# Performance work log

Hardware: AMD Instinct MI355X
Metric: run time of the kernel (lower is better)

## Reference

```python
import jax, jax.numpy as jnp
import numpy as np

N = 50000      # nodes
E = 800000     # edges
G = 512        # graphs
H = 256        # hidden_dim
T = 32         # tag embedding dim
L = 4          # num_layers
EPS = 1e-5


def setup_inputs() -> dict:
    key = jax.random.key(0)
    ks = jax.random.split(key, 16)
    x = jax.random.randint(ks[0], (N,), 0, 100)
    tags = jax.random.randint(ks[1], (N,), 0, 3)
    edge_index = jax.random.randint(ks[2], (2, E), 0, N)
    batch = jnp.sort(jax.random.randint(ks[3], (N,), 0, G))
    s = 1.0 / np.sqrt(H)
    atom_emb = jax.random.normal(ks[4], (100, H), jnp.float32)
    tag_emb = jax.random.normal(ks[5], (3, T), jnp.float32)
    Wp = jax.random.normal(ks[6], (H + T, H), jnp.float32) * (1.0 / np.sqrt(H + T))
    bp = jnp.zeros((H,), jnp.float32)
    gcn_W = jax.random.normal(ks[7], (L, H, H), jnp.float32) * s
    gcn_b = jnp.zeros((L, H), jnp.float32)
    bn_g = jnp.ones((L, H), jnp.float32)
    bn_b = jnp.zeros((L, H), jnp.float32)
    W1 = jax.random.normal(ks[8], (H, H // 2), jnp.float32) * s
    b1 = jnp.zeros((H // 2,), jnp.float32)
    W2 = jax.random.normal(ks[9], (H // 2, 1), jnp.float32) * (1.0 / np.sqrt(H // 2))
    b2 = jnp.zeros((1,), jnp.float32)
    return dict(x=x, tags=tags, edge_index=edge_index, batch=batch,
                atom_emb=atom_emb, tag_emb=tag_emb, Wp=Wp, bp=bp,
                gcn_W=gcn_W, gcn_b=gcn_b, bn_g=bn_g, bn_b=bn_b,
                W1=W1, b1=b1, W2=W2, b2=b2)


def _gcn_conv(h, W, b, src, dst, dinv):
    # PyG GCNConv: x' = W x, symmetric normalization with self-loops.
    hw = h @ W                                   # [N, H]
    norm = dinv[src] * dinv[dst]                 # [E]
    msg = hw[src] * norm[:, None]                # [E, H]  (gather)
    agg = jax.ops.segment_sum(msg, dst, num_segments=N)  # scatter-add
    agg = agg + hw * (dinv * dinv)[:, None]      # self-loop term
    return agg + b


def _batch_norm(x, g, b):
    mu = jnp.mean(x, axis=0)
    var = jnp.var(x, axis=0)
    return (x - mu) * jax.lax.rsqrt(var + EPS) * g + b


def reference(x, tags, edge_index, batch, atom_emb, tag_emb, Wp, bp,
              gcn_W, gcn_b, bn_g, bn_b, W1, b1, W2, b2):
    src, dst = edge_index[0], edge_index[1]
    # degree with self-loops (gcn_norm counts on the dst/col index)
    deg = jax.ops.segment_sum(jnp.ones((E,), jnp.float32), dst, num_segments=N) + 1.0
    dinv = jax.lax.rsqrt(deg)

    h = jnp.concatenate([atom_emb[x], tag_emb[tags]], axis=1) @ Wp + bp  # [N, H]
    for l in range(L):
        res = h
        h = _gcn_conv(h, gcn_W[l], gcn_b[l], src, dst, dinv)
        h = jax.nn.relu(_batch_norm(h, bn_g[l], bn_b[l]))
        h = h + res                                  # dropout is identity in eval

    # global mean pool over graphs
    sums = jax.ops.segment_sum(h, batch, num_segments=G)
    cnts = jax.ops.segment_sum(jnp.ones((N,), jnp.float32), batch, num_segments=G)
    pooled = sums / jnp.maximum(cnts, 1.0)[:, None]  # [G, H]

    hid = jax.nn.relu(pooled @ W1 + b1)
    energy = hid @ W2 + b2                           # [G, 1]
    return energy.squeeze(-1)
```

## Files before the change

### kernel.cpp

```cpp
#include <hip/hip_runtime.h>
#include <hip/hip_bf16.h>

#define NN 50000
#define EE 800000
#define GG 512
#define HH 256
#define TT 32
#define LL 4
#define EPSF 1e-5f

typedef __attribute__((ext_vector_type(8))) short short8;
typedef __attribute__((ext_vector_type(4))) float float4v;

__device__ inline unsigned short f2b(float f) {
    unsigned u = __float_as_uint(f);
    unsigned r = (u + 0x7FFFu + ((u >> 16) & 1u)) >> 16;
    return (unsigned short)r;
}
__device__ inline float4 bf4_to_f4(ushort4 u) {
    float4 f;
    f.x = __uint_as_float((unsigned)u.x << 16);
    f.y = __uint_as_float((unsigned)u.y << 16);
    f.z = __uint_as_float((unsigned)u.z << 16);
    f.w = __uint_as_float((unsigned)u.w << 16);
    return f;
}

__global__ void k_degree(const int* __restrict__ dst, int* __restrict__ cnt, int E) {
    int e = blockIdx.x * 256 + threadIdx.x;
    if (e < E) atomicAdd(&cnt[dst[e]], 1);
}

__global__ void k_dinv(const int* __restrict__ cnt, float* __restrict__ dinv, int N) {
    int i = blockIdx.x * 256 + threadIdx.x;
    if (i < N) dinv[i] = rsqrtf((float)cnt[i] + 1.0f);
}

__global__ void k_scan1(const int* __restrict__ cnt, int* __restrict__ incl,
                        int* __restrict__ bsum, int N) {
    __shared__ int s[1024];
    int i = blockIdx.x * 1024 + threadIdx.x;
    int v = (i < N) ? cnt[i] : 0;
    s[threadIdx.x] = v;
    __syncthreads();
    for (int off = 1; off < 1024; off <<= 1) {
        int t = (threadIdx.x >= off) ? s[threadIdx.x - off] : 0;
        __syncthreads();
        s[threadIdx.x] += t;
        __syncthreads();
    }
    if (i < N) incl[i] = s[threadIdx.x];
    if (threadIdx.x == 1023) bsum[blockIdx.x] = s[1023];
}

__global__ void k_scan2(int* __restrict__ bsum, int nb) {
    __shared__ int s[64];
    int v = (threadIdx.x < nb) ? bsum[threadIdx.x] : 0;
    s[threadIdx.x] = v;
    __syncthreads();
    for (int off = 1; off < 64; off <<= 1) {
        int t = (threadIdx.x >= off) ? s[threadIdx.x - off] : 0;
        __syncthreads();
        s[threadIdx.x] += t;
        __syncthreads();
    }
    if (threadIdx.x < nb) bsum[threadIdx.x] = s[threadIdx.x] - v;
}

__global__ void k_scan3(int* __restrict__ rs, const int* __restrict__ cnt,
                        const int* __restrict__ boff, int N) {
    int i = blockIdx.x * 256 + threadIdx.x;
    if (i < N) rs[i] = rs[i] + boff[i >> 10] - cnt[i];
}

__global__ void k_scatter(const int* __restrict__ src, const int* __restrict__ dst,
                          const int* __restrict__ rs, int* __restrict__ cur,
                          int* __restrict__ csr, int E) {
    int e = blockIdx.x * 256 + threadIdx.x;
    if (e >= E) return;
    int d = dst[e];
    int p = rs[d] + atomicAdd(&cur[d], 1);
    csr[p] = src[e];
}

__global__ void k_wprep(const float* __restrict__ W, unsigned short* __restrict__ Wt) {
    int l = blockIdx.y;
    int n = blockIdx.x * 4 + (threadIdx.x >> 6);
    int kq = (threadIdx.x & 63) * 4;
    const float* Wl = W + (size_t)l * HH * HH;
    ushort4 o;
    o.x = f2b(Wl[(size_t)(kq + 0) * HH + n]);
    o.y = f2b(Wl[(size_t)(kq + 1) * HH + n]);
    o.z = f2b(Wl[(size_t)(kq + 2) * HH + n]);
    o.w = f2b(Wl[(size_t)(kq + 3) * HH + n]);
    *(ushort4*)(Wt + (size_t)l * HH * HH + (size_t)n * HH + kq) = o;
}

__global__ void k_proj(const float* __restrict__ atom_emb, const float* __restrict__ tag_emb,
                       const float* __restrict__ Wp, const float* __restrict__ bp,
                       float* __restrict__ aref, float* __restrict__ tref) {
    int r = blockIdx.x;
    int j = threadIdx.x;
    if (r < 100) {
        float acc = bp[j];
        for (int k = 0; k < HH; ++k) acc += atom_emb[r * HH + k] * Wp[(size_t)k * HH + j];
        aref[r * HH + j] = acc;
    } else {
        int tr = r - 100;
        float acc = 0.f;
        for (int k = 0; k < TT; ++k) acc += tag_emb[tr * TT + k] * Wp[(size_t)(HH + k) * HH + j];
        tref[tr * HH + j] = acc;
    }
}

__global__ void k_h0(const int* __restrict__ x, const int* __restrict__ tags,
                     const float* __restrict__ aref, const float* __restrict__ tref,
                     float* __restrict__ h, unsigned short* __restrict__ hb, int N) {
    int n = blockIdx.x;
    int lane = threadIdx.x;
    float4 a = ((const float4*)(aref + (size_t)x[n] * HH))[lane];
    float4 t = ((const float4*)(tref + (size_t)tags[n] * HH))[lane];
    float4 r;
    r.x = a.x + t.x; r.y = a.y + t.y; r.z = a.z + t.z; r.w = a.w + t.w;
    ((float4*)(h + (size_t)n * HH))[lane] = r;
    ushort4 u;
    u.x = f2b(r.x); u.y = f2b(r.y); u.z = f2b(r.z); u.w = f2b(r.w);
    ((ushort4*)(hb + (size_t)n * HH))[lane] = u;
}

__global__ __launch_bounds__(256) void k_gemm(const unsigned short* __restrict__ hb,
                                              const unsigned short* __restrict__ Wt,
                                              const float* __restrict__ dinv,
                                              unsigned short* __restrict__ hwb, int M) {
    __shared__ unsigned short As[128][72];
    __shared__ unsigned short Bs[128][72];
    int t = threadIdx.x;
    int lane = t & 63, w = t >> 6;
    int wr = w >> 1, wc = w & 1;
    int l15 = lane & 15, l4 = lane >> 4;
    int row0 = blockIdx.y * 128, col0 = blockIdx.x * 128;
    float4v acc[4][4];
#pragma unroll
    for (int i = 0; i < 4; ++i)
#pragma unroll
        for (int j = 0; j < 4; ++j) acc[i][j] = (float4v)0.f;

    for (int k0 = 0; k0 < 256; k0 += 64) {
        if (k0) __syncthreads();
#pragma unroll
        for (int u = 0; u < 4; ++u) {
            int idx = u * 256 + t;
            int r = idx >> 3;
            int c = (idx & 7) * 8;
            *(uint4*)&As[r][c] = *(const uint4*)(hb + (size_t)(row0 + r) * 256 + k0 + c);
            *(uint4*)&Bs[r][c] = *(const uint4*)(Wt + (size_t)(col0 + r) * 256 + k0 + c);
        }
        __syncthreads();
#pragma unroll
        for (int kk = 0; kk < 64; kk += 32) {
            short8 a[4], b[4];
#pragma unroll
            for (int i = 0; i < 4; ++i)
                a[i] = *(const short8*)&As[wr * 64 + i * 16 + l15][kk + l4 * 8];
#pragma unroll
            for (int i = 0; i < 4; ++i)
                b[i] = *(const short8*)&Bs[wc * 64 + i * 16 + l15][kk + l4 * 8];
#pragma unroll
            for (int mi = 0; mi < 4; ++mi)
#pragma unroll
                for (int ni = 0; ni < 4; ++ni)
                    acc[mi][ni] = __builtin_amdgcn_mfma_f32_16x16x32_bf16(
                        a[mi], b[ni], acc[mi][ni], 0, 0, 0);
        }
    }
#pragma unroll
    for (int mi = 0; mi < 4; ++mi) {
        int mb = row0 + wr * 64 + mi * 16 + l4 * 4;
        float dv[4];
#pragma unroll
        for (int r = 0; r < 4; ++r) dv[r] = (mb + r < M) ? dinv[mb + r] : 0.f;
#pragma unroll
        for (int ni = 0; ni < 4; ++ni) {
            int n = col0 + wc * 64 + ni * 16 + l15;
#pragma unroll
            for (int r = 0; r < 4; ++r) {
                if (mb + r < M)
                    hwb[(size_t)(mb + r) * 256 + n] = f2b(acc[mi][ni][r] * dv[r]);
            }
        }
    }
}

__global__ void k_agg(const unsigned short* __restrict__ hwb, float* __restrict__ agg,
                      const int* __restrict__ csr, const int* __restrict__ rs,
                      const int* __restrict__ cnt, const float* __restrict__ dinv,
                      const float* __restrict__ bias, int N) {
    int wave = threadIdx.x >> 6;
    int lane = threadIdx.x & 63;
    int n = blockIdx.x * 4 + wave;
    if (n >= N) return;
    float dn = dinv[n];
    int e = rs[n];
    int end = e + cnt[n];
    float4 acc = bf4_to_f4(((const ushort4*)(hwb + (size_t)n * HH))[lane]);
    for (; e + 4 <= end; e += 4) {
        int s0 = csr[e], s1 = csr[e + 1], s2 = csr[e + 2], s3 = csr[e + 3];
        float4 m0 = bf4_to_f4(((const ushort4*)(hwb + (size_t)s0 * HH))[lane]);
        float4 m1 = bf4_to_f4(((const ushort4*)(hwb + (size_t)s1 * HH))[lane]);
        float4 m2 = bf4_to_f4(((const ushort4*)(hwb + (size_t)s2 * HH))[lane]);
        float4 m3 = bf4_to_f4(((const ushort4*)(hwb + (size_t)s3 * HH))[lane]);
        acc.x += (m0.x + m1.x) + (m2.x + m3.x);
        acc.y += (m0.y + m1.y) + (m2.y + m3.y);
        acc.z += (m0.z + m1.z) + (m2.z + m3.z);
        acc.w += (m0.w + m1.w) + (m2.w + m3.w);
    }
    for (; e < end; ++e) {
        int s = csr[e];
        float4 m = bf4_to_f4(((const ushort4*)(hwb + (size_t)s * HH))[lane]);
        acc.x += m.x; acc.y += m.y; acc.z += m.z; acc.w += m.w;
    }
    float4 b = ((const float4*)bias)[lane];
    float4 r;
    r.x = acc.x * dn + b.x; r.y = acc.y * dn + b.y;
    r.z = acc.z * dn + b.z; r.w = acc.w * dn + b.w;
    ((float4*)(agg + (size_t)n * HH))[lane] = r;
}

__global__ __launch_bounds__(256) void k_bnstats(const float4* __restrict__ agg,
                                                 float* __restrict__ colsum,
                                                 float* __restrict__ colsq, int N) {
    __shared__ float4 ssum[4][64];
    __shared__ float4 ssq[4][64];
    int lane = threadIdx.x & 63;
    int wv = threadIdx.x >> 6;
    int rows_per = (N + gridDim.x - 1) / gridDim.x;
    int r0 = blockIdx.x * rows_per;
    int r1 = r0 + rows_per; if (r1 > N) r1 = N;
    float4 s = make_float4(0.f, 0.f, 0.f, 0.f);
    float4 s2 = make_float4(0.f, 0.f, 0.f, 0.f);
    for (int r = r0 + wv; r < r1; r += 4) {
        float4 v = agg[(size_t)r * 64 + lane];
        s.x += v.x; s.y += v.y; s.z += v.z; s.w += v.w;
        s2.x += v.x * v.x; s2.y += v.y * v.y; s2.z += v.z * v.z; s2.w += v.w * v.w;
    }
    ssum[wv][lane] = s;
    ssq[wv][lane] = s2;
    __syncthreads();
    int j = lane * 4;
    if (wv == 0) {
        float4 a = ssum[0][lane], b = ssum[1][lane], c = ssum[2][lane], d = ssum[3][lane];
        atomicAdd(&colsum[j + 0], a.x + b.x + c.x + d.x);
        atomicAdd(&colsum[j + 1], a.y + b.y + c.y + d.y);
        atomicAdd(&colsum[j + 2], a.z + b.z + c.z + d.z);
        atomicAdd(&colsum[j + 3], a.w + b.w + c.w + d.w);
    } else if (wv == 1) {
        float4 a = ssq[0][lane], b = ssq[1][lane], c = ssq[2][lane], d = ssq[3][lane];
        atomicAdd(&colsq[j + 0], a.x + b.x + c.x + d.x);
        atomicAdd(&colsq[j + 1], a.y + b.y + c.y + d.y);
        atomicAdd(&colsq[j + 2], a.z + b.z + c.z + d.z);
        atomicAdd(&colsq[j + 3], a.w + b.w + c.w + d.w);
    }
}

__global__ void k_epi(const float4* __restrict__ agg, float4* __restrict__ h,
                      ushort4* __restrict__ hb,
                      const float4* __restrict__ colsum, const float4* __restrict__ colsq,
                      const float4* __restrict__ g4, const float4* __restrict__ b4,
                      int total, float invN) {
    int idx = blockIdx.x * 256 + threadIdx.x;
    if (idx >= total) return;
    int q = idx & 63;
    float4 a = agg[idx];
    float4 s = colsum[q], s2 = colsq[q], g = g4[q], b = b4[q];
    float4 hv = h[idx];
    float mu, var, v;
    mu = s.x * invN; var = s2.x * invN - mu * mu;
    v = (a.x - mu) * rsqrtf(var + EPSF) * g.x + b.x; hv.x += fmaxf(v, 0.f);
    mu = s.y * invN; var = s2.y * invN - mu * mu;
    v = (a.y - mu) * rsqrtf(var + EPSF) * g.y + b.y; hv.y += fmaxf(v, 0.f);
    mu = s.z * invN; var = s2.z * invN - mu * mu;
    v = (a.z - mu) * rsqrtf(var + EPSF) * g.z + b.z; hv.z += fmaxf(v, 0.f);
    mu = s.w * invN; var = s2.w * invN - mu * mu;
    v = (a.w - mu) * rsqrtf(var + EPSF) * g.w + b.w; hv.w += fmaxf(v, 0.f);
    h[idx] = hv;
    ushort4 u;
    u.x = f2b(hv.x); u.y = f2b(hv.y); u.z = f2b(hv.z); u.w = f2b(hv.w);
    hb[idx] = u;
}

__global__ void k_ginit(int* __restrict__ gstart, int G, int N) {
    int g = blockIdx.x * 256 + threadIdx.x;
    if (g <= G) gstart[g] = N;
}

__global__ void k_gbound(const int* __restrict__ batch, int* __restrict__ gstart, int N) {
    int n = blockIdx.x * 256 + threadIdx.x;
    if (n >= N) return;
    int b = batch[n];
    int prev = (n == 0) ? -1 : batch[n - 1];
    for (int g = prev + 1; g <= b; ++g) gstart[g] = n;
}

__global__ void k_pool(const float4* __restrict__ h, const int* __restrict__ gstart,
                       float* __restrict__ pooled) {
    __shared__ float4 sm[4][64];
    int g = blockIdx.x;
    int t = threadIdx.x;
    int lane = t & 63, wv = t >> 6;
    int s = gstart[g], e = gstart[g + 1];
    float4 acc = make_float4(0.f, 0.f, 0.f, 0.f);
    for (int n = s + wv; n < e; n += 4) {
        float4 v = h[(size_t)n * 64 + lane];
        acc.x += v.x; acc.y += v.y; acc.z += v.z; acc.w += v.w;
    }
    sm[wv][lane] = acc;
    __syncthreads();
    if (wv == 0) {
        float4 a = sm[0][lane], b = sm[1][lane], c = sm[2][lane], d = sm[3][lane];
        float inv = 1.0f / fmaxf((float)(e - s), 1.0f);
        float4 r;
        r.x = (a.x + b.x + c.x + d.x) * inv;
        r.y = (a.y + b.y + c.y + d.y) * inv;
        r.z = (a.z + b.z + c.z + d.z) * inv;
        r.w = (a.w + b.w + c.w + d.w) * inv;
        ((float4*)pooled)[(size_t)g * 64 + lane] = r;
    }
}

__global__ void k_head(const float* __restrict__ pooled,
                       const float* __restrict__ W1, const float* __restrict__ b1,
                       const float* __restrict__ W2, const float* __restrict__ b2,
                       float* __restrict__ out) {
    __shared__ float prow[256];
    __shared__ float hred[128];
    int g = blockIdx.x, t = threadIdx.x;
    prow[t] = pooled[(size_t)g * HH + t];
    prow[t + 128] = pooled[(size_t)g * HH + t + 128];
    __syncthreads();
    float acc = b1[t];
    for (int k = 0; k < HH; ++k) acc += prow[k] * W1[(size_t)k * 128 + t];
    float hid = fmaxf(acc, 0.f);
    hred[t] = hid * W2[t];
    __syncthreads();
    for (int off = 64; off > 0; off >>= 1) {
        if (t < off) hred[t] += hred[t + off];
        __syncthreads();
    }
    if (t == 0) out[g] = hred[0] + b2[0];
}

extern "C" void kernel_launch(void* const* d_in, const int* in_sizes, int n_in,
                              void* d_out, int out_size, void* d_ws, size_t ws_size,
                              hipStream_t stream) {
    const int* x        = (const int*)d_in[0];
    const int* tags     = (const int*)d_in[1];
    const int* ei       = (const int*)d_in[2];
    const int* batch    = (const int*)d_in[3];
    const float* atom_e = (const float*)d_in[4];
    const float* tag_e  = (const float*)d_in[5];
    const float* Wp     = (const float*)d_in[6];
    const float* bp     = (const float*)d_in[7];
    const float* gcn_W  = (const float*)d_in[8];
    const float* gcn_b  = (const float*)d_in[9];
    const float* bn_g   = (const float*)d_in[10];
    const float* bn_b   = (const float*)d_in[11];
    const float* W1     = (const float*)d_in[12];
    const float* b1     = (const float*)d_in[13];
    const float* W2     = (const float*)d_in[14];
    const float* b2     = (const float*)d_in[15];
    float* out = (float*)d_out;

    const int N = NN, E = EE, G = GG, H = HH;
    const int Mpad = ((N + 127) / 128) * 128;

    char* p = (char*)d_ws;
    auto alloc = [&](size_t bytes) {
        void* r = (void*)p;
        p += (bytes + 255) & ~(size_t)255;
        return r;
    };
    float* h    = (float*)alloc((size_t)N * H * 4);
    unsigned short* hb  = (unsigned short*)alloc((size_t)Mpad * H * 2);
    unsigned short* hwb = (unsigned short*)alloc((size_t)Mpad * H * 2);
    unsigned short* Wt  = (unsigned short*)alloc((size_t)LL * H * H * 2);
    float* agg  = (float*)alloc((size_t)N * H * 4);
    float* dinv = (float*)alloc((size_t)N * 4);
    int* cnt    = (int*)alloc((size_t)N * 4);
    int* rs     = (int*)alloc((size_t)N * 4);
    int* cur    = (int*)alloc((size_t)N * 4);
    int* csr    = (int*)alloc((size_t)E * 4);
    int* bsum   = (int*)alloc(64 * 4);
    float* aref = (float*)alloc(100 * (size_t)H * 4);
    float* tref = (float*)alloc(3 * (size_t)H * 4);
    float* cstat= (float*)alloc(2 * (size_t)H * 4);
    int* gstart = (int*)alloc((size_t)(G + 1) * 4);
    float* pooled = (float*)alloc((size_t)G * H * 4);

    const int* src = ei;
    const int* dst = ei + E;

    hipMemsetAsync(cnt, 0, (size_t)N * 4, stream);
    hipMemsetAsync(cur, 0, (size_t)N * 4, stream);

    k_degree<<<(E + 255) / 256, 256, 0, stream>>>(dst, cnt, E);
    k_dinv<<<(N + 255) / 256, 256, 0, stream>>>(cnt, dinv, N);

    int nb = (N + 1023) / 1024;
    k_scan1<<<nb, 1024, 0, stream>>>(cnt, rs, bsum, N);
    k_scan2<<<1, 64, 0, stream>>>(bsum, nb);
    k_scan3<<<(N + 255) / 256, 256, 0, stream>>>(rs, cnt, bsum, N);
    k_scatter<<<(E + 255) / 256, 256, 0, stream>>>(src, dst, rs, cur, csr, E);

    k_ginit<<<(G + 256) / 256, 256, 0, stream>>>(gstart, G, N);
    k_gbound<<<(N + 255) / 256, 256, 0, stream>>>(batch, gstart, N);

    k_wprep<<<dim3(64, LL), 256, 0, stream>>>(gcn_W, Wt);
    k_proj<<<103, 256, 0, stream>>>(atom_e, tag_e, Wp, bp, aref, tref);
    k_h0<<<N, 64, 0, stream>>>(x, tags, aref, tref, h, hb, N);

    for (int l = 0; l < LL; ++l) {
        k_gemm<<<dim3(2, Mpad / 128), 256, 0, stream>>>(
            hb, Wt + (size_t)l * H * H, dinv, hwb, N);
        k_agg<<<(N + 3) / 4, 256, 0, stream>>>(hwb, agg, csr, rs, cnt, dinv,
                                               gcn_b + (size_t)l * H, N);
        hipMemsetAsync(cstat, 0, 2 * (size_t)H * 4, stream);
        k_bnstats<<<512, 256, 0, stream>>>((const float4*)agg, cstat, cstat + H, N);
        k_epi<<<(N * 64 + 255) / 256, 256, 0, stream>>>(
            (const float4*)agg, (float4*)h, (ushort4*)hb,
            (const float4*)cstat, (const float4*)(cstat + H),
            (const float4*)(bn_g + (size_t)l * H), (const float4*)(bn_b + (size_t)l * H),
            N * 64, 1.0f / (float)N);
    }

    k_pool<<<G, 256, 0, stream>>>((const float4*)h, gstart, pooled);
    k_head<<<G, 128, 0, stream>>>(pooled, W1, b1, W2, b2, out);
}
```

Measured before the change: 941.8 us.

## Drop fp32 residual buffer, keep hidden state in bf16; unroll aggregation by eight

Removes the fp32 hidden-state array so the residual and pooling read the bf16 copy hb directly. This cuts a 51 MB fp32 read and write per layer in the epilogue, plus the fp32 writes in the initial embedding kernel. The neighbour aggregation loop also gains an 8-way unrolled path to keep more gather loads in flight. The trade-off is that the residual now accumulates in bf16 across layers, which loses precision.

```diff
diff --git a/kernel.cpp b/kernel.cpp
--- a/kernel.cpp
+++ b/kernel.cpp
@@ -115,16 +115,14 @@
 
 __global__ void k_h0(const int* __restrict__ x, const int* __restrict__ tags,
                      const float* __restrict__ aref, const float* __restrict__ tref,
-                     float* __restrict__ h, unsigned short* __restrict__ hb, int N) {
+                     unsigned short* __restrict__ hb, int N) {
     int n = blockIdx.x;
     int lane = threadIdx.x;
     float4 a = ((const float4*)(aref + (size_t)x[n] * HH))[lane];
     float4 t = ((const float4*)(tref + (size_t)tags[n] * HH))[lane];
-    float4 r;
-    r.x = a.x + t.x; r.y = a.y + t.y; r.z = a.z + t.z; r.w = a.w + t.w;
-    ((float4*)(h + (size_t)n * HH))[lane] = r;
     ushort4 u;
-    u.x = f2b(r.x); u.y = f2b(r.y); u.z = f2b(r.z); u.w = f2b(r.w);
+    u.x = f2b(a.x + t.x); u.y = f2b(a.y + t.y);
+    u.z = f2b(a.z + t.z); u.w = f2b(a.w + t.w);
     ((ushort4*)(hb + (size_t)n * HH))[lane] = u;
 }
 
@@ -203,6 +201,22 @@
     int e = rs[n];
     int end = e + cnt[n];
     float4 acc = bf4_to_f4(((const ushort4*)(hwb + (size_t)n * HH))[lane]);
+    for (; e + 8 <= end; e += 8) {
+        int s0 = csr[e],     s1 = csr[e + 1], s2 = csr[e + 2], s3 = csr[e + 3];
+        int s4 = csr[e + 4], s5 = csr[e + 5], s6 = csr[e + 6], s7 = csr[e + 7];
+        float4 m0 = bf4_to_f4(((const ushort4*)(hwb + (size_t)s0 * HH))[lane]);
+        float4 m1 = bf4_to_f4(((const ushort4*)(hwb + (size_t)s1 * HH))[lane]);
+        float4 m2 = bf4_to_f4(((const ushort4*)(hwb + (size_t)s2 * HH))[lane]);
+        float4 m3 = bf4_to_f4(((const ushort4*)(hwb + (size_t)s3 * HH))[lane]);
+        float4 m4 = bf4_to_f4(((const ushort4*)(hwb + (size_t)s4 * HH))[lane]);
+        float4 m5 = bf4_to_f4(((const ushort4*)(hwb + (size_t)s5 * HH))[lane]);
+        float4 m6 = bf4_to_f4(((const ushort4*)(hwb + (size_t)s6 * HH))[lane]);
+        float4 m7 = bf4_to_f4(((const ushort4*)(hwb + (size_t)s7 * HH))[lane]);
+        acc.x += ((m0.x + m1.x) + (m2.x + m3.x)) + ((m4.x + m5.x) + (m6.x + m7.x));
+        acc.y += ((m0.y + m1.y) + (m2.y + m3.y)) + ((m4.y + m5.y) + (m6.y + m7.y));
+        acc.z += ((m0.z + m1.z) + (m2.z + m3.z)) + ((m4.z + m5.z) + (m6.z + m7.z));
+        acc.w += ((m0.w + m1.w) + (m2.w + m3.w)) + ((m4.w + m5.w) + (m6.w + m7.w));
+    }
     for (; e + 4 <= end; e += 4) {
         int s0 = csr[e], s1 = csr[e + 1], s2 = csr[e + 2], s3 = csr[e + 3];
         float4 m0 = bf4_to_f4(((const ushort4*)(hwb + (size_t)s0 * HH))[lane]);
@@ -262,8 +276,7 @@
     }
 }
 
-__global__ void k_epi(const float4* __restrict__ agg, float4* __restrict__ h,
-                      ushort4* __restrict__ hb,
+__global__ void k_epi(const float4* __restrict__ agg, ushort4* __restrict__ hb,
                       const float4* __restrict__ colsum, const float4* __restrict__ colsq,
                       const float4* __restrict__ g4, const float4* __restrict__ b4,
                       int total, float invN) {
@@ -272,7 +285,7 @@
     int q = idx & 63;
     float4 a = agg[idx];
     float4 s = colsum[q], s2 = colsq[q], g = g4[q], b = b4[q];
-    float4 hv = h[idx];
+    float4 hv = bf4_to_f4(hb[idx]);
     float mu, var, v;
     mu = s.x * invN; var = s2.x * invN - mu * mu;
     v = (a.x - mu) * rsqrtf(var + EPSF) * g.x + b.x; hv.x += fmaxf(v, 0.f);
@@ -282,7 +295,6 @@
     v = (a.z - mu) * rsqrtf(var + EPSF) * g.z + b.z; hv.z += fmaxf(v, 0.f);
     mu = s.w * invN; var = s2.w * invN - mu * mu;
     v = (a.w - mu) * rsqrtf(var + EPSF) * g.w + b.w; hv.w += fmaxf(v, 0.f);
-    h[idx] = hv;
     ushort4 u;
     u.x = f2b(hv.x); u.y = f2b(hv.y); u.z = f2b(hv.z); u.w = f2b(hv.w);
     hb[idx] = u;
@@ -301,7 +313,7 @@
     for (int g = prev + 1; g <= b; ++g) gstart[g] = n;
 }
 
-__global__ void k_pool(const float4* __restrict__ h, const int* __restrict__ gstart,
+__global__ void k_pool(const unsigned short* __restrict__ hb, const int* __restrict__ gstart,
                        float* __restrict__ pooled) {
     __shared__ float4 sm[4][64];
     int g = blockIdx.x;
@@ -310,7 +322,7 @@
     int s = gstart[g], e = gstart[g + 1];
     float4 acc = make_float4(0.f, 0.f, 0.f, 0.f);
     for (int n = s + wv; n < e; n += 4) {
-        float4 v = h[(size_t)n * 64 + lane];
+        float4 v = bf4_to_f4(((const ushort4*)(hb + (size_t)n * HH))[lane]);
         acc.x += v.x; acc.y += v.y; acc.z += v.z; acc.w += v.w;
     }
     sm[wv][lane] = acc;
@@ -379,7 +391,6 @@
         p += (bytes + 255) & ~(size_t)255;
         return r;
     };
-    float* h    = (float*)alloc((size_t)N * H * 4);
     unsigned short* hb  = (unsigned short*)alloc((size_t)Mpad * H * 2);
     unsigned short* hwb = (unsigned short*)alloc((size_t)Mpad * H * 2);
     unsigned short* Wt  = (unsigned short*)alloc((size_t)LL * H * H * 2);
@@ -416,7 +427,7 @@
 
     k_wprep<<<dim3(64, LL), 256, 0, stream>>>(gcn_W, Wt);
     k_proj<<<103, 256, 0, stream>>>(atom_e, tag_e, Wp, bp, aref, tref);
-    k_h0<<<N, 64, 0, stream>>>(x, tags, aref, tref, h, hb, N);
+    k_h0<<<N, 64, 0, stream>>>(x, tags, aref, tref, hb, N);
 
     for (int l = 0; l < LL; ++l) {
         k_gemm<<<dim3(2, Mpad / 128), 256, 0, stream>>>(
@@ -426,12 +437,12 @@
         hipMemsetAsync(cstat, 0, 2 * (size_t)H * 4, stream);
         k_bnstats<<<512, 256, 0, stream>>>((const float4*)agg, cstat, cstat + H, N);
         k_epi<<<(N * 64 + 255) / 256, 256, 0, stream>>>(
-            (const float4*)agg, (float4*)h, (ushort4*)hb,
+            (const float4*)agg, (ushort4*)hb,
             (const float4*)cstat, (const float4*)(cstat + H),
             (const float4*)(bn_g + (size_t)l * H), (const float4*)(bn_b + (size_t)l * H),
             N * 64, 1.0f / (float)N);
     }
 
-    k_pool<<<G, 256, 0, stream>>>((const float4*)h, gstart, pooled);
+    k_pool<<<G, 256, 0, stream>>>(hb, gstart, pooled);
     k_head<<<G, 128, 0, stream>>>(pooled, W1, b1, W2, b2, out);
 }
```

Result: faster. 899.9 us (-4.4%).
